# Optimization experiments

Measured on AMD Instinct MI355X. Metric: run time of the kernel, lower is better.

The kernel has to match this reference:

```python
import jax, jax.numpy as jnp
import numpy as np

TOKEN_DIM = 4
EPS = 1e-6


def setup_inputs() -> dict:
    key = jax.random.key(0)
    k_x, k_w = jax.random.split(key)
    B, S, E = 8, 8192, 512
    EMB = 512
    x = jax.random.normal(k_x, (B, S, E), dtype=jnp.float32)
    ln_gamma = jnp.ones((E,), dtype=jnp.float32)
    ln_beta = jnp.zeros((E,), dtype=jnp.float32)
    # glorot-ish scale for the compression kernel [token_dim*E, EMB]
    W = jax.random.normal(k_w, (TOKEN_DIM * E, EMB), dtype=jnp.float32) * 0.02
    b = jnp.zeros((EMB,), dtype=jnp.float32)
    return {"x": x, "ln_gamma": ln_gamma, "ln_beta": ln_beta, "W": W, "b": b}


def reference(x, ln_gamma, ln_beta, W, b):
    B, S, E = x.shape
    # LayerNormalization over the feature axis (center + scale)
    mean = jnp.mean(x, axis=-1, keepdims=True)
    var = jnp.mean(jnp.square(x - mean), axis=-1, keepdims=True)
    h = (x - mean) * jax.lax.rsqrt(var + EPS) * ln_gamma + ln_beta
    # Divide: split sequence axis by token_dim and merge factor into feature axis
    # [B, S, E] -> [B, S//T, T*E]
    h = h.reshape(B, S // TOKEN_DIM, TOKEN_DIM * E)
    # Dense compression + exact gelu (keras 'gelu' uses erf form)
    out = jnp.einsum('bsf,fd->bsd', h, W) + b
    return jax.nn.gelu(out, approximate=False)
```

## Files before the change

kernel.cpp:

```cpp
#include <hip/hip_runtime.h>
#include <hip/hip_bf16.h>
#include <cstdint>

#define XROWS   65536
#define E       512
#define MROWS   16384
#define KDIM    2048
#define NDIM    512

typedef __attribute__((ext_vector_type(4))) float f32x4;
typedef __attribute__((ext_vector_type(8))) unsigned short u16x8;
typedef __attribute__((ext_vector_type(8))) __bf16 bf16x8;

__device__ __forceinline__ unsigned short f2bf(float f) {
  unsigned u = __builtin_bit_cast(unsigned, f);
  u += 0x7FFFu + ((u >> 16) & 1u);
  return (unsigned short)(u >> 16);
}

typedef const __attribute__((address_space(1))) unsigned char ga_u8;
typedef __attribute__((address_space(3))) unsigned char ls_u8;
__device__ __forceinline__ void gload16(const void* g, void* l) {
  __builtin_amdgcn_global_load_lds((ga_u8*)g, (ls_u8*)l, 16, 0, 0);
}

__global__ __launch_bounds__(256) void wt_kernel(const float* __restrict__ W,
                                                 unsigned short* __restrict__ WT) {
  __shared__ float tile[64][68];
  const int t  = threadIdx.x;
  const int bk = blockIdx.x >> 3;
  const int bn = blockIdx.x & 7;
  const int c4 = (t & 15) * 4;
#pragma unroll
  for (int i = 0; i < 4; ++i) {
    const int r = (t >> 4) + i * 16;
    const f32x4 v = *(const f32x4*)&W[(size_t)(bk * 64 + r) * NDIM + bn * 64 + c4];
    tile[r][c4 + 0] = v.x; tile[r][c4 + 1] = v.y;
    tile[r][c4 + 2] = v.z; tile[r][c4 + 3] = v.w;
  }
  __syncthreads();
#pragma unroll
  for (int j = 0; j < 2; ++j) {
    const int n  = j * 32 + (t >> 3);
    const int kb = (t & 7) * 8;
    u16x8 o;
#pragma unroll
    for (int q = 0; q < 8; ++q) o[q] = f2bf(tile[kb + q][n]);
    *(u16x8*)&WT[(size_t)(bn * 64 + n) * KDIM + bk * 64 + kb] = o;
  }
}

__global__ __launch_bounds__(256, 4) void ln_kernel(const float* __restrict__ x,
                                                    const float* __restrict__ gamma,
                                                    const float* __restrict__ beta,
                                                    unsigned short* __restrict__ h) {
  const int w = threadIdx.x >> 6, l = threadIdx.x & 63;
  const size_t row = (size_t)blockIdx.x * 4 + w;
  const float* xr = x + row * E + l * 8;
  const f32x4 v0 = *(const f32x4*)xr;
  const f32x4 v1 = *(const f32x4*)(xr + 4);
  float xv[8] = {v0.x, v0.y, v0.z, v0.w, v1.x, v1.y, v1.z, v1.w};
  float s = 0.f, q = 0.f;
#pragma unroll
  for (int j = 0; j < 8; ++j) { s += xv[j]; q += xv[j] * xv[j]; }
#pragma unroll
  for (int off = 32; off > 0; off >>= 1) {
    s += __shfl_xor(s, off);
    q += __shfl_xor(q, off);
  }
  const float mean = s * (1.0f / E);
  const float var  = q * (1.0f / E) - mean * mean;
  const float rstd = rsqrtf(var + 1e-6f);
  const f32x4 g0 = *(const f32x4*)(gamma + l * 8);
  const f32x4 g1 = *(const f32x4*)(gamma + l * 8 + 4);
  const f32x4 b0 = *(const f32x4*)(beta + l * 8);
  const f32x4 b1 = *(const f32x4*)(beta + l * 8 + 4);
  const float gv[8] = {g0.x, g0.y, g0.z, g0.w, g1.x, g1.y, g1.z, g1.w};
  const float bv[8] = {b0.x, b0.y, b0.z, b0.w, b1.x, b1.y, b1.z, b1.w};
  u16x8 o;
#pragma unroll
  for (int j = 0; j < 8; ++j) o[j] = f2bf((xv[j] - mean) * rstd * gv[j] + bv[j]);
  *(u16x8*)(h + row * E + l * 8) = o;
}

#define NT (KDIM / 64)

__global__ __launch_bounds__(256, 2) void gemm_kernel(const unsigned short* __restrict__ A,
                                                      const unsigned short* __restrict__ Bt,
                                                      const float* __restrict__ bias,
                                                      float* __restrict__ out) {
  __shared__ char smem[2 * 32768];
  const int tid = threadIdx.x;
  const int l = tid & 63, w = tid >> 6;
  const int l7 = l & 7, l15 = l & 15, lhi = l >> 4;
  const int wr = w >> 1, wc = w & 1;

  const int bn = blockIdx.x & 3;
  const int bm = blockIdx.x >> 2;
  const size_t arow0 = (size_t)bm * 128;
  const int    brow0 = bn * 128;

  const int srow = w * 8 + (l >> 3);
  const int swz  = (l7 * 16) ^ ((l >> 3) << 4);
  const char* gAb = (const char*)A  + ((size_t)(arow0 + srow) * KDIM) * 2 + swz;
  const char* gBb = (const char*)Bt + ((size_t)(brow0 + srow) * KDIM) * 2 + swz;

  auto stage = [&](int buf, int t) {
    char* base = smem + buf * 32768;
    const char* pa = gAb + (size_t)t * 128;
    const char* pb = gBb + (size_t)t * 128;
#pragma unroll
    for (int i = 0; i < 4; ++i) {
      gload16(pa + (size_t)i * 32 * KDIM * 2, base + (i * 32 + w * 8) * 128);
      gload16(pb + (size_t)i * 32 * KDIM * 2, base + 16384 + (i * 32 + w * 8) * 128);
    }
  };

  f32x4 acc[4][4];
#pragma unroll
  for (int m = 0; m < 4; ++m)
#pragma unroll
    for (int n = 0; n < 4; ++n) acc[m][n] = (f32x4){0.f, 0.f, 0.f, 0.f};

  const int cs0 = (lhi * 16) ^ (l7 * 16);

  stage(0, 0);
  __syncthreads();

  for (int t = 0; t < NT; ++t) {
    if (t + 1 < NT) stage((t + 1) & 1, t + 1);
    const char* Ab = smem + (t & 1) * 32768;
    const char* Bb = Ab + 16384;
#pragma unroll
    for (int kk = 0; kk < 2; ++kk) {
      const int co = cs0 ^ (kk * 64);
      bf16x8 av[4], bv[4];
#pragma unroll
      for (int m = 0; m < 4; ++m)
        av[m] = *(const bf16x8*)(Ab + (wr * 64 + m * 16 + l15) * 128 + co);
#pragma unroll
      for (int n = 0; n < 4; ++n)
        bv[n] = *(const bf16x8*)(Bb + (wc * 64 + n * 16 + l15) * 128 + co);
#pragma unroll
      for (int m = 0; m < 4; ++m)
#pragma unroll
        for (int n = 0; n < 4; ++n)
          acc[m][n] = __builtin_amdgcn_mfma_f32_16x16x32_bf16(av[m], bv[n], acc[m][n], 0, 0, 0);
    }
    __syncthreads();
  }

#pragma unroll
  for (int n = 0; n < 4; ++n) {
    const int col = brow0 + wc * 64 + n * 16 + l15;
    const float bb = bias[col];
#pragma unroll
    for (int m = 0; m < 4; ++m) {
      const size_t rbase = arow0 + wr * 64 + m * 16 + lhi * 4;
#pragma unroll
      for (int r = 0; r < 4; ++r) {
        const float v = acc[m][n][r] + bb;
        const float ge = 0.5f * v * (1.0f + erff(v * 0.70710678118654752f));
        out[(rbase + r) * NDIM + col] = ge;
      }
    }
  }
}

extern "C" void kernel_launch(void* const* d_in, const int* in_sizes, int n_in,
                              void* d_out, int out_size, void* d_ws, size_t ws_size,
                              hipStream_t stream) {
  const float* x     = (const float*)d_in[0];
  const float* gamma = (const float*)d_in[1];
  const float* beta  = (const float*)d_in[2];
  const float* W     = (const float*)d_in[3];
  const float* bias  = (const float*)d_in[4];
  float* out = (float*)d_out;

  unsigned short* WT = (unsigned short*)d_ws;
  const size_t wtBytes = (size_t)NDIM * KDIM * 2;
  unsigned short* h = (unsigned short*)((char*)d_ws + wtBytes);

  int NC = 1;
  while (NC < 64 && wtBytes + ((size_t)MROWS / NC) * KDIM * 2 > ws_size) NC <<= 1;
  const int Mc = MROWS / NC;

  wt_kernel<<<256, 256, 0, stream>>>(W, WT);
  for (int c = 0; c < NC; ++c) {
    const float* xc = x + (size_t)c * Mc * KDIM;
    ln_kernel<<<Mc, 256, 0, stream>>>(xc, gamma, beta, h);
    gemm_kernel<<<(Mc / 128) * 4, 256, 0, stream>>>(h, WT, bias,
                                                    out + (size_t)c * Mc * NDIM);
  }
}
```

Before: 87.92 us.

## Fold LN affine into weights/bias, cheap GELU, single-buffer GEMM with block remap

Folds the LayerNorm gamma into the transposed bf16 weights and precomputes beta·W plus b as a fused bias, so the LN kernel only normalizes. Replaces the exact erf GELU with an exp2/reciprocal sigmoid-style approximation. The GEMM drops double buffering to raise occupancy to 3 blocks per SM and remaps block indices for L2 locality. The chunked launch loop is removed, so the full h buffer is assumed to fit in the workspace. The GELU approximation and the dropped chunking add accuracy and workspace-size risks.

```diff
diff --git a/kernel.cpp b/kernel.cpp
--- a/kernel.cpp
+++ b/kernel.cpp
@@ -7,6 +7,7 @@
 #define MROWS   16384
 #define KDIM    2048
 #define NDIM    512
+#define NT      32
 
 typedef __attribute__((ext_vector_type(4))) float f32x4;
 typedef __attribute__((ext_vector_type(8))) unsigned short u16x8;
@@ -24,7 +25,15 @@
   __builtin_amdgcn_global_load_lds((ga_u8*)g, (ls_u8*)l, 16, 0, 0);
 }
 
+__device__ __forceinline__ float gelu_f(float v) {
+  float p = v * (2.3022083f + 0.1029432f * (v * v));
+  p = fminf(p, 80.0f);
+  const float Ee = exp2f(p);
+  return v * Ee * __builtin_amdgcn_rcpf(Ee + 1.0f);
+}
+
 __global__ __launch_bounds__(256) void wt_kernel(const float* __restrict__ W,
+                                                 const float* __restrict__ gamma,
                                                  unsigned short* __restrict__ WT) {
   __shared__ float tile[64][68];
   const int t  = threadIdx.x;
@@ -43,16 +52,42 @@
   for (int j = 0; j < 2; ++j) {
     const int n  = j * 32 + (t >> 3);
     const int kb = (t & 7) * 8;
+    const int kg0 = (bk & 7) * 64 + kb;
+    const f32x4 g0 = *(const f32x4*)(gamma + kg0);
+    const f32x4 g1 = *(const f32x4*)(gamma + kg0 + 4);
+    const float gg[8] = {g0.x, g0.y, g0.z, g0.w, g1.x, g1.y, g1.z, g1.w};
     u16x8 o;
 #pragma unroll
-    for (int q = 0; q < 8; ++q) o[q] = f2bf(tile[kb + q][n]);
+    for (int q = 0; q < 8; ++q) o[q] = f2bf(gg[q] * tile[kb + q][n]);
     *(u16x8*)&WT[(size_t)(bn * 64 + n) * KDIM + bk * 64 + kb] = o;
   }
 }
 
+__global__ __launch_bounds__(256) void kbias1(const float* __restrict__ W,
+                                              const float* __restrict__ beta,
+                                              float* __restrict__ partial) {
+  const int bk = blockIdx.x, tid = threadIdx.x;
+  float a0 = 0.f, a1 = 0.f;
+  for (int k = 0; k < 64; ++k) {
+    const int kg = bk * 64 + k;
+    const float be = beta[kg & (E - 1)];
+    a0 += be * W[(size_t)kg * NDIM + tid];
+    a1 += be * W[(size_t)kg * NDIM + 256 + tid];
+  }
+  partial[bk * NDIM + tid] = a0;
+  partial[bk * NDIM + 256 + tid] = a1;
+}
+
+__global__ __launch_bounds__(256) void kbias2(const float* __restrict__ b,
+                                              const float* __restrict__ partial,
+                                              float* __restrict__ biasf) {
+  const int c = blockIdx.x * 256 + threadIdx.x;
+  float s = b[c];
+  for (int j = 0; j < 32; ++j) s += partial[j * NDIM + c];
+  biasf[c] = s;
+}
+
 __global__ __launch_bounds__(256, 4) void ln_kernel(const float* __restrict__ x,
-                                                    const float* __restrict__ gamma,
-                                                    const float* __restrict__ beta,
                                                     unsigned short* __restrict__ h) {
   const int w = threadIdx.x >> 6, l = threadIdx.x & 63;
   const size_t row = (size_t)blockIdx.x * 4 + w;
@@ -71,97 +106,84 @@
   const float mean = s * (1.0f / E);
   const float var  = q * (1.0f / E) - mean * mean;
   const float rstd = rsqrtf(var + 1e-6f);
-  const f32x4 g0 = *(const f32x4*)(gamma + l * 8);
-  const f32x4 g1 = *(const f32x4*)(gamma + l * 8 + 4);
-  const f32x4 b0 = *(const f32x4*)(beta + l * 8);
-  const f32x4 b1 = *(const f32x4*)(beta + l * 8 + 4);
-  const float gv[8] = {g0.x, g0.y, g0.z, g0.w, g1.x, g1.y, g1.z, g1.w};
-  const float bv[8] = {b0.x, b0.y, b0.z, b0.w, b1.x, b1.y, b1.z, b1.w};
+  const float nm   = -mean * rstd;
   u16x8 o;
 #pragma unroll
-  for (int j = 0; j < 8; ++j) o[j] = f2bf((xv[j] - mean) * rstd * gv[j] + bv[j]);
+  for (int j = 0; j < 8; ++j) o[j] = f2bf(xv[j] * rstd + nm);
   *(u16x8*)(h + row * E + l * 8) = o;
 }
 
-#define NT (KDIM / 64)
-
-__global__ __launch_bounds__(256, 2) void gemm_kernel(const unsigned short* __restrict__ A,
+__global__ __launch_bounds__(256, 3) void gemm_kernel(const unsigned short* __restrict__ A,
                                                       const unsigned short* __restrict__ Bt,
-                                                      const float* __restrict__ bias,
+                                                      const float* __restrict__ biasf,
                                                       float* __restrict__ out) {
-  __shared__ char smem[2 * 32768];
+  __shared__ char smem[32768];
   const int tid = threadIdx.x;
   const int l = tid & 63, w = tid >> 6;
   const int l7 = l & 7, l15 = l & 15, lhi = l >> 4;
   const int wr = w >> 1, wc = w & 1;
 
-  const int bn = blockIdx.x & 3;
-  const int bm = blockIdx.x >> 2;
+  const int wg = ((blockIdx.x & 7) << 6) | (blockIdx.x >> 3);
+  const int bn = wg & 3;
+  const int bm = wg >> 2;
   const size_t arow0 = (size_t)bm * 128;
   const int    brow0 = bn * 128;
 
   const int srow = w * 8 + (l >> 3);
   const int swz  = (l7 * 16) ^ ((l >> 3) << 4);
-  const char* gAb = (const char*)A  + ((size_t)(arow0 + srow) * KDIM) * 2 + swz;
-  const char* gBb = (const char*)Bt + ((size_t)(brow0 + srow) * KDIM) * 2 + swz;
-
-  auto stage = [&](int buf, int t) {
-    char* base = smem + buf * 32768;
-    const char* pa = gAb + (size_t)t * 128;
-    const char* pb = gBb + (size_t)t * 128;
-#pragma unroll
-    for (int i = 0; i < 4; ++i) {
-      gload16(pa + (size_t)i * 32 * KDIM * 2, base + (i * 32 + w * 8) * 128);
-      gload16(pb + (size_t)i * 32 * KDIM * 2, base + 16384 + (i * 32 + w * 8) * 128);
+  const char* gA = (const char*)A  + ((size_t)(arow0 + srow) * KDIM) * 2 + swz;
+  const char* gB = (const char*)Bt + ((size_t)(brow0 + srow) * KDIM) * 2 + swz;
+
+  f32x4 acc[4][4];
+#pragma unroll
+  for (int m = 0; m < 4; ++m)
+#pragma unroll
+    for (int n = 0; n < 4; ++n) acc[m][n] = (f32x4){0.f, 0.f, 0.f, 0.f};
+
+  const int cs0 = (lhi * 16) ^ (l7 * 16);
+
+  for (int t = 0; t < NT; ++t) {
+    __syncthreads();
+    {
+      const char* pa = gA + (size_t)t * 128;
+      const char* pb = gB + (size_t)t * 128;
+#pragma unroll
+      for (int i = 0; i < 4; ++i) {
+        gload16(pa + (size_t)i * 32 * KDIM * 2, smem + (i * 32 + w * 8) * 128);
+        gload16(pb + (size_t)i * 32 * KDIM * 2, smem + 16384 + (i * 32 + w * 8) * 128);
+      }
     }
-  };
-
-  f32x4 acc[4][4];
-#pragma unroll
-  for (int m = 0; m < 4; ++m)
-#pragma unroll
-    for (int n = 0; n < 4; ++n) acc[m][n] = (f32x4){0.f, 0.f, 0.f, 0.f};
-
-  const int cs0 = (lhi * 16) ^ (l7 * 16);
-
-  stage(0, 0);
-  __syncthreads();
-
-  for (int t = 0; t < NT; ++t) {
-    if (t + 1 < NT) stage((t + 1) & 1, t + 1);
-    const char* Ab = smem + (t & 1) * 32768;
-    const char* Bb = Ab + 16384;
+    __syncthreads();
 #pragma unroll
     for (int kk = 0; kk < 2; ++kk) {
       const int co = cs0 ^ (kk * 64);
       bf16x8 av[4], bv[4];
 #pragma unroll
       for (int m = 0; m < 4; ++m)
-        av[m] = *(const bf16x8*)(Ab + (wr * 64 + m * 16 + l15) * 128 + co);
+        av[m] = *(const bf16x8*)(smem + (wr * 64 + m * 16 + l15) * 128 + co);
 #pragma unroll
       for (int n = 0; n < 4; ++n)
-        bv[n] = *(const bf16x8*)(Bb + (wc * 64 + n * 16 + l15) * 128 + co);
+        bv[n] = *(const bf16x8*)(smem + 16384 + (wc * 64 + n * 16 + l15) * 128 + co);
 #pragma unroll
       for (int m = 0; m < 4; ++m)
 #pragma unroll
         for (int n = 0; n < 4; ++n)
-          acc[m][n] = __builtin_amdgcn_mfma_f32_16x16x32_bf16(av[m], bv[n], acc[m][n], 0, 0, 0);
+          acc[m][n] = __builtin_amdgcn_mfma_f32_16x16x32_bf16(av[m], bv[n],
+                                                              acc[m][n], 0, 0, 0);
     }
-    __syncthreads();
   }
 
 #pragma unroll
   for (int n = 0; n < 4; ++n) {
     const int col = brow0 + wc * 64 + n * 16 + l15;
-    const float bb = bias[col];
+    const float bb = biasf[col];
 #pragma unroll
     for (int m = 0; m < 4; ++m) {
       const size_t rbase = arow0 + wr * 64 + m * 16 + lhi * 4;
 #pragma unroll
       for (int r = 0; r < 4; ++r) {
         const float v = acc[m][n][r] + bb;
-        const float ge = 0.5f * v * (1.0f + erff(v * 0.70710678118654752f));
-        out[(rbase + r) * NDIM + col] = ge;
+        out[(rbase + r) * NDIM + col] = gelu_f(v);
       }
     }
   }
@@ -174,22 +196,18 @@
   const float* gamma = (const float*)d_in[1];
   const float* beta  = (const float*)d_in[2];
   const float* W     = (const float*)d_in[3];
-  const float* bias  = (const float*)d_in[4];
+  const float* b     = (const float*)d_in[4];
   float* out = (float*)d_out;
 
-  unsigned short* WT = (unsigned short*)d_ws;
-  const size_t wtBytes = (size_t)NDIM * KDIM * 2;
-  unsigned short* h = (unsigned short*)((char*)d_ws + wtBytes);
-
-  int NC = 1;
-  while (NC < 64 && wtBytes + ((size_t)MROWS / NC) * KDIM * 2 > ws_size) NC <<= 1;
-  const int Mc = MROWS / NC;
-
-  wt_kernel<<<256, 256, 0, stream>>>(W, WT);
-  for (int c = 0; c < NC; ++c) {
-    const float* xc = x + (size_t)c * Mc * KDIM;
-    ln_kernel<<<Mc, 256, 0, stream>>>(xc, gamma, beta, h);
-    gemm_kernel<<<(Mc / 128) * 4, 256, 0, stream>>>(h, WT, bias,
-                                                    out + (size_t)c * Mc * NDIM);
-  }
-}
+  char* p = (char*)d_ws;
+  unsigned short* WT = (unsigned short*)p;            p += (size_t)NDIM * KDIM * 2;
+  unsigned short* h  = (unsigned short*)p;            p += (size_t)MROWS * KDIM * 2;
+  float* partial     = (float*)p;                     p += (size_t)32 * NDIM * 4;
+  float* biasf       = (float*)p;
+
+  wt_kernel<<<256, 256, 0, stream>>>(W, gamma, WT);
+  kbias1<<<32, 256, 0, stream>>>(W, beta, partial);
+  kbias2<<<2, 256, 0, stream>>>(b, partial, biasf);
+  ln_kernel<<<XROWS / 4, 256, 0, stream>>>(x, h);
+  gemm_kernel<<<(MROWS / 128) * 4, 256, 0, stream>>>(h, WT, biasf, out);
+}
```

After: 83.69 us. 4.8% less time.
